# Performance work log

Measured on AMD Instinct MI355X. Metric: run time of the kernel, lower is better.

## Reference

```python
import jax, jax.numpy as jnp
import numpy as np

NUM_EXPERTS = 8
TOP_K = 2
HIDDEN = 2048
INTER = 7168
B, S = 4, 2048


def setup_inputs() -> dict:
    key = jax.random.key(0)
    k0, k1, k2, k3, k4 = jax.random.split(key, 5)
    scale_h = 1.0 / np.sqrt(HIDDEN)
    scale_i = 1.0 / np.sqrt(INTER)
    return {
        "hidden_states": jax.random.normal(k0, (B, S, HIDDEN), dtype=jnp.float32),
        "gate_w": jax.random.normal(k1, (NUM_EXPERTS, HIDDEN), dtype=jnp.float32) * scale_h,
        "w1": jax.random.normal(k2, (NUM_EXPERTS, INTER, HIDDEN), dtype=jnp.float32) * scale_h,
        "w3": jax.random.normal(k3, (NUM_EXPERTS, INTER, HIDDEN), dtype=jnp.float32) * scale_h,
        "w2": jax.random.normal(k4, (NUM_EXPERTS, HIDDEN, INTER), dtype=jnp.float32) * scale_i,
    }


def reference(hidden_states, gate_w, w1, w3, w2):
    orig_shape = hidden_states.shape
    x = hidden_states.reshape(-1, HIDDEN)              # [T, H]

    # Router: gate linear -> softmax -> top-k -> renormalize.
    router_logits = x @ gate_w.T                       # [T, E]
    probs = jax.nn.softmax(router_logits, axis=-1)
    topk_w, topk_idx = jax.lax.top_k(probs, TOP_K)     # [T, K]
    topk_w = topk_w / jnp.sum(topk_w, axis=-1, keepdims=True)

    # Dense combine weights: [T, E] with top-k renormalized weights scattered.
    combine = jnp.sum(
        jax.nn.one_hot(topk_idx, NUM_EXPERTS, dtype=x.dtype) * topk_w[..., None],
        axis=1,
    )                                                   # [T, E]

    out = jnp.zeros_like(x)
    # Fixed small loop over experts (structurally distinct weight matrices);
    # avoids materializing a [T, E, I] intermediate.
    for e in range(NUM_EXPERTS):
        g = jax.nn.silu(x @ w1[e].T)                   # [T, I]
        u = x @ w3[e].T                                # [T, I]
        y = (g * u) @ w2[e].T                          # [T, H]
        out = out + combine[:, e:e + 1] * y

    return out.reshape(orig_shape)
```

## Files before the change

### kernel.cpp

```cpp
#include <hip/hip_runtime.h>
#include <stdint.h>

#define NE    8
#define HID   2048
#define INTER 7168
#define TTOK  8192
#define NT1   (HID / 64)
#define NT2   (INTER / 64)

typedef __bf16 bf16;
typedef bf16 bf16x4 __attribute__((ext_vector_type(4)));
typedef bf16 bf16x8 __attribute__((ext_vector_type(8)));
typedef float f32x4 __attribute__((ext_vector_type(4)));

__device__ __forceinline__ void glds16(const void* g, void* l) {
  __builtin_amdgcn_global_load_lds((__attribute__((address_space(1))) void*)g,
                                   (__attribute__((address_space(3))) void*)l, 16, 0, 0);
}

__global__ void cvt_f32_bf16(const float* __restrict__ src, bf16* __restrict__ dst, long n) {
  long i = (long)blockIdx.x * blockDim.x + threadIdx.x;
  long stride = (long)gridDim.x * blockDim.x;
  for (long j = i * 4; j < n; j += stride * 4) {
    float4 v = *(const float4*)(src + j);
    bf16x4 o = {(bf16)v.x, (bf16)v.y, (bf16)v.z, (bf16)v.w};
    *(bf16x4*)(dst + j) = o;
  }
}

__global__ void router_kernel(const float* __restrict__ x, const float* __restrict__ gw,
                              int* __restrict__ topk_e, float* __restrict__ topk_w) {
  const int wid = threadIdx.x >> 6, lane = threadIdx.x & 63;
  const int t = blockIdx.x * 4 + wid;
  if (t >= TTOK) return;
  const float* xr = x + (size_t)t * HID;
  float xv[32];
#pragma unroll
  for (int i = 0; i < 32; ++i) xv[i] = xr[lane + 64 * i];
  float lg[NE];
#pragma unroll
  for (int e = 0; e < NE; ++e) {
    const float* g = gw + e * HID;
    float s = 0.f;
#pragma unroll
    for (int i = 0; i < 32; ++i) s += xv[i] * g[lane + 64 * i];
#pragma unroll
    for (int off = 32; off; off >>= 1) s += __shfl_down(s, off);
    lg[e] = s;
  }
  if (lane == 0) {
    int i1 = 0;
#pragma unroll
    for (int e = 1; e < NE; ++e) if (lg[e] > lg[i1]) i1 = e;
    int i2 = (i1 == 0) ? 1 : 0;
#pragma unroll
    for (int e = 0; e < NE; ++e) if (e != i2 && e != i1 && lg[e] > lg[i2]) i2 = e;
    float r = __expf(lg[i2] - lg[i1]);
    float wa = 1.f / (1.f + r);
    topk_e[2 * t] = i1; topk_e[2 * t + 1] = i2;
    topk_w[2 * t] = wa; topk_w[2 * t + 1] = 1.f - wa;
  }
}

__global__ void gather_sorted(const int* __restrict__ topk_e, const float* __restrict__ topk_w,
                              int* __restrict__ cnt, int* __restrict__ ltok,
                              float* __restrict__ lw, int* __restrict__ ppos) {
  const int e = blockIdx.x;
  const int tid = threadIdx.x;
  const int lane = tid & 63, wv = tid >> 6;
  __shared__ int wtot[4];
  __shared__ int basesh;
  if (tid == 0) basesh = 0;
  __syncthreads();
  for (int c0 = 0; c0 < TTOK; c0 += 256) {
    const int t = c0 + tid;
    const int e0 = topk_e[2 * t], e1 = topk_e[2 * t + 1];
    const int j = (e0 == e) ? 0 : 1;
    const int flag = (e0 == e) || (e1 == e);
    unsigned long long b = __ballot(flag);
    int wrank = __popcll(b & ((1ULL << lane) - 1ULL));
    if (lane == 63) wtot[wv] = __popcll(b);
    __syncthreads();
    int wbase = 0;
#pragma unroll
    for (int k = 0; k < 4; ++k) if (k < wv) wbase += wtot[k];
    const int total = wtot[0] + wtot[1] + wtot[2] + wtot[3];
    const int pos = basesh + wbase + wrank;
    if (flag) {
      ltok[e * TTOK + pos] = t;
      lw[e * TTOK + pos] = (j == 0) ? topk_w[2 * t] : topk_w[2 * t + 1];
      ppos[2 * t + j] = pos;
    }
    __syncthreads();
    if (tid == 0) basesh += total;
    __syncthreads();
  }
  if (tid == 0) cnt[e] = basesh;
}

__global__ void prefix_kernel(const int* __restrict__ cnt, int* __restrict__ base) {
  if (threadIdx.x == 0 && blockIdx.x == 0) {
    int b = 0;
    for (int e = 0; e < NE; ++e) { base[e] = b; b += cnt[e]; }
    base[NE] = b;
  }
}

__global__ void combine_kernel(const float* __restrict__ ybuf, const int* __restrict__ topk_e,
                               const int* __restrict__ ppos, const int* __restrict__ basep,
                               float* __restrict__ out) {
  const int t = blockIdx.x;
  const int col = threadIdx.x * 8;
  const int g0 = basep[topk_e[2 * t]] + ppos[2 * t];
  const int g1 = basep[topk_e[2 * t + 1]] + ppos[2 * t + 1];
  const float4* y0 = (const float4*)(ybuf + (size_t)g0 * HID + col);
  const float4* y1 = (const float4*)(ybuf + (size_t)g1 * HID + col);
  float4* o = (float4*)(out + (size_t)t * HID + col);
  float4 a0 = y0[0], b0 = y1[0];
  float4 a1 = y0[1], b1 = y1[1];
  o[0] = make_float4(a0.x + b0.x, a0.y + b0.y, a0.z + b0.z, a0.w + b0.w);
  o[1] = make_float4(a1.x + b1.x, a1.y + b1.y, a1.z + b1.z, a1.w + b1.w);
}


#define MFMA(a, b, c) __builtin_amdgcn_mfma_f32_16x16x32_bf16((a), (b), (c), 0, 0, 0)

#define STAGE_A(h, kt) do { int _b = ((kt) & 1) * 32768; size_t _k = (size_t)(kt) * 128; \
    glds16(bA + oA[(h)*2 + 0] + _k, ldsA + _b + (h) * 16384 + d0); \
    glds16(bA + oA[(h)*2 + 1] + _k, ldsA + _b + (h) * 16384 + d1); } while (0)
#define STAGE_B(h, kt) do { int _b = ((kt) & 1) * 32768; size_t _k = (size_t)(kt) * 128; \
    glds16(bB + oB[(h)*2 + 0] + _k, ldsB + _b + (h) * 16384 + d0); \
    glds16(bB + oB[(h)*2 + 1] + _k, ldsB + _b + (h) * 16384 + d1); } while (0)

#define RD_A(mf, ks) (*(const bf16x8*)(ldsA + curb + arow + (mf) * (16 * 128) + ((ks) ? kcol1 : kcol0)))
#define RD_B(nf, ks) (*(const bf16x8*)(ldsB + curb + brow + (nf) * (16 * 128) + ((ks) ? kcol1 : kcol0)))

#define BAR()    __builtin_amdgcn_s_barrier()
#define LGKMC(n) do { asm volatile("s_waitcnt lgkmcnt(" #n ")" ::: "memory"); \
                      __builtin_amdgcn_sched_barrier(0); } while (0)
#define SCHED0() __builtin_amdgcn_sched_barrier(0)

#define Q_MFMA(AM, BM, ACCM, ACCN_OFF) do { \
  __builtin_amdgcn_s_setprio(1); \
  _Pragma("unroll") \
  for (int m = 0; m < 4; ++m) \
    _Pragma("unroll") \
    for (int n = 0; n < 2; ++n) { \
      acc[ACCM + m][ACCN_OFF + n] = MFMA(AM[m][0], BM[n][0], acc[ACCM + m][ACCN_OFF + n]); \
      acc[ACCM + m][ACCN_OFF + n] = MFMA(AM[m][1], BM[n][1], acc[ACCM + m][ACCN_OFF + n]); \
    } \
  __builtin_amdgcn_s_setprio(0); \
} while (0)

__launch_bounds__(512, 2)
__global__ void pass1_kernel(const bf16* __restrict__ xb, const bf16* __restrict__ w1b,
                             bf16* __restrict__ hbuf, const int* __restrict__ cnt,
                             const int* __restrict__ basep, const int* __restrict__ ltok) {
  const int e = blockIdx.z;
  const int c = cnt[e];
  const int tm = blockIdx.y;
  if (tm * 256 >= c) return;
  const int tn = blockIdx.x;

  __shared__ __align__(16) bf16 sA[2][256 * 64];
  __shared__ __align__(16) bf16 sB[2][256 * 64];
  char* const ldsA = (char*)&sA[0][0];
  char* const ldsB = (char*)&sB[0][0];

  const int tid = threadIdx.x;
  const int r0 = tid >> 3;
  const int ls = (tid & 7) ^ (r0 & 7);
  const int d0 = tid * 16, d1 = (tid + 512) * 16;
  const char* const bA = (const char*)xb;
  const char* const bB = (const char*)w1b;

  uint32_t oA[4], oB[4];
#pragma unroll
  for (int i = 0; i < 4; ++i) {
    int trow = i * 64 + r0;
    int slot = tm * 256 + trow; if (slot >= c) slot = c - 1;
    oA[i] = (uint32_t)((size_t)ltok[e * TTOK + slot] * (HID * 2) + ls * 16);
    int br = i * 64 + r0;
    int w = (br >> 4) & 1;
    int wr = tn * 128 + ((br >> 5) << 4) + (br & 15);
    size_t off = ((size_t)e * INTER + wr) * (HID * 2) + (size_t)ls * 16;
    if (w) off += (size_t)NE * INTER * HID * 2;
    oB[i] = (uint32_t)off;
  }

  const int lane = tid & 63, wid = tid >> 6;
  const int wm = wid >> 2, wn = wid & 3;
  const int ln15 = lane & 15, kq = lane >> 4;
  const int swz = (ln15 & 7) << 4;
  const int kcol0 = (kq * 16) ^ swz;
  const int kcol1 = (64 + kq * 16) ^ swz;
  const int arow = (wm * 128 + ln15) * 128;
  const int brow = (wn * 64 + ln15) * 128;

  f32x4 acc[8][4];
#pragma unroll
  for (int m = 0; m < 8; ++m)
#pragma unroll
    for (int n = 0; n < 4; ++n) acc[m][n] = (f32x4){0.f, 0.f, 0.f, 0.f};

  STAGE_A(0, 0); STAGE_A(1, 0); STAGE_B(0, 0); STAGE_B(1, 0);
  asm volatile("s_waitcnt vmcnt(4)" ::: "memory");
  STAGE_A(0, 1); STAGE_A(1, 1); STAGE_B(0, 1);
  asm volatile("s_waitcnt vmcnt(6)" ::: "memory");
  BAR();

  bf16x8 a0[4][2], a1[4][2], b0[2][2], b1[2][2];
  int cur = 0;
  for (int t = 0; t < NT1; ++t, cur ^= 1) {
    const int curb = cur * 32768;
#pragma unroll
    for (int m = 0; m < 4; ++m) { a0[m][0] = RD_A(m, 0); a0[m][1] = RD_A(m, 1); }
#pragma unroll
    for (int n = 0; n < 2; ++n) { b0[n][0] = RD_B(n, 0); b0[n][1] = RD_B(n, 1); }
    if (t + 1 < NT1) STAGE_B(1, t + 1);
    BAR(); LGKMC(12);
    if (t > 0) Q_MFMA(a1, b1, 4, 2);
    BAR();
#pragma unroll
    for (int m = 0; m < 4; ++m) { a1[m][0] = RD_A(4 + m, 0); a1[m][1] = RD_A(4 + m, 1); }
    BAR(); LGKMC(8);
    Q_MFMA(a0, b0, 0, 0);
    BAR();
#pragma unroll
    for (int n = 0; n < 2; ++n) { b1[n][0] = RD_B(2 + n, 0); b1[n][1] = RD_B(2 + n, 1); }
    if (t + 2 < NT1) { STAGE_A(0, t + 2); STAGE_A(1, t + 2); SCHED0(); }
    BAR(); LGKMC(4);
    Q_MFMA(a1, b0, 4, 0);
    BAR();
    if (t + 2 < NT1) STAGE_B(0, t + 2);
    LGKMC(0);
    Q_MFMA(a0, b1, 0, 2);
    if (t + 2 < NT1) asm volatile("s_waitcnt vmcnt(6)" ::: "memory");
    else             asm volatile("s_waitcnt vmcnt(0)" ::: "memory");
    BAR();
  }
  Q_MFMA(a1, b1, 4, 2);

  const int be = basep[e];
#pragma unroll
  for (int mh = 0; mh < 2; ++mh)
#pragma unroll
    for (int mf = 0; mf < 4; ++mf)
#pragma unroll
      for (int j = 0; j < 4; ++j) {
        const int slot = tm * 256 + wm * 128 + mh * 64 + mf * 16 + kq * 4 + j;
        if (slot < c) {
          bf16* hrow = hbuf + (size_t)(be + slot) * INTER + tn * 128;
#pragma unroll
          for (int p = 0; p < 2; ++p) {
            const float g = acc[mh * 4 + mf][2 * p][j];
            const float u = acc[mh * 4 + mf][2 * p + 1][j];
            const float hv = g / (1.f + __expf(-g)) * u;
            hrow[wn * 32 + p * 16 + ln15] = (bf16)hv;
          }
        }
      }
}

__launch_bounds__(512, 2)
__global__ void pass2_kernel(const bf16* __restrict__ hbuf, const bf16* __restrict__ w2b,
                             float* __restrict__ ybuf, const int* __restrict__ cnt,
                             const int* __restrict__ basep, const float* __restrict__ lw) {
  const int e = blockIdx.z;
  const int c = cnt[e];
  const int tm = blockIdx.y;
  if (tm * 256 >= c) return;
  const int tn = blockIdx.x;

  __shared__ __align__(16) bf16 sA[2][256 * 64];
  __shared__ __align__(16) bf16 sB[2][256 * 64];
  char* const ldsA = (char*)&sA[0][0];
  char* const ldsB = (char*)&sB[0][0];

  const int tid = threadIdx.x;
  const int r0 = tid >> 3;
  const int ls = (tid & 7) ^ (r0 & 7);
  const int d0 = tid * 16, d1 = (tid + 512) * 16;
  const int be = basep[e];
  const char* const bA = (const char*)hbuf;
  const char* const bB = (const char*)w2b;

  uint32_t oA[4], oB[4];
#pragma unroll
  for (int i = 0; i < 4; ++i) {
    int trow = i * 64 + r0;
    int slot = tm * 256 + trow; if (slot >= c) slot = c - 1;
    oA[i] = (uint32_t)((size_t)(be + slot) * (INTER * 2) + ls * 16);
    oB[i] = (uint32_t)(((size_t)e * HID + tn * 256 + i * 64 + r0) * (INTER * 2) + (size_t)ls * 16);
  }

  const int lane = tid & 63, wid = tid >> 6;
  const int wm = wid >> 2, wn = wid & 3;
  const int ln15 = lane & 15, kq = lane >> 4;
  const int swz = (ln15 & 7) << 4;
  const int kcol0 = (kq * 16) ^ swz;
  const int kcol1 = (64 + kq * 16) ^ swz;
  const int arow = (wm * 128 + ln15) * 128;
  const int brow = (wn * 64 + ln15) * 128;

  f32x4 acc[8][4];
#pragma unroll
  for (int m = 0; m < 8; ++m)
#pragma unroll
    for (int n = 0; n < 4; ++n) acc[m][n] = (f32x4){0.f, 0.f, 0.f, 0.f};

  STAGE_A(0, 0); STAGE_A(1, 0); STAGE_B(0, 0); STAGE_B(1, 0);
  asm volatile("s_waitcnt vmcnt(4)" ::: "memory");
  STAGE_A(0, 1); STAGE_A(1, 1); STAGE_B(0, 1);
  asm volatile("s_waitcnt vmcnt(6)" ::: "memory");
  BAR();

  bf16x8 a0[4][2], a1[4][2], b0[2][2], b1[2][2];
  int cur = 0;
  for (int t = 0; t < NT2; ++t, cur ^= 1) {
    const int curb = cur * 32768;
#pragma unroll
    for (int m = 0; m < 4; ++m) { a0[m][0] = RD_A(m, 0); a0[m][1] = RD_A(m, 1); }
#pragma unroll
    for (int n = 0; n < 2; ++n) { b0[n][0] = RD_B(n, 0); b0[n][1] = RD_B(n, 1); }
    if (t + 1 < NT2) STAGE_B(1, t + 1);
    BAR(); LGKMC(12);
    if (t > 0) Q_MFMA(a1, b1, 4, 2);
    BAR();
#pragma unroll
    for (int m = 0; m < 4; ++m) { a1[m][0] = RD_A(4 + m, 0); a1[m][1] = RD_A(4 + m, 1); }
    BAR(); LGKMC(8);
    Q_MFMA(a0, b0, 0, 0);
    BAR();
#pragma unroll
    for (int n = 0; n < 2; ++n) { b1[n][0] = RD_B(2 + n, 0); b1[n][1] = RD_B(2 + n, 1); }
    if (t + 2 < NT2) { STAGE_A(0, t + 2); STAGE_A(1, t + 2); SCHED0(); }
    BAR(); LGKMC(4);
    Q_MFMA(a1, b0, 4, 0);
    BAR();
    if (t + 2 < NT2) STAGE_B(0, t + 2);
    LGKMC(0);
    Q_MFMA(a0, b1, 0, 2);
    if (t + 2 < NT2) asm volatile("s_waitcnt vmcnt(6)" ::: "memory");
    else             asm volatile("s_waitcnt vmcnt(0)" ::: "memory");
    BAR();
  }
  Q_MFMA(a1, b1, 4, 2);

#pragma unroll
  for (int mh = 0; mh < 2; ++mh)
#pragma unroll
    for (int mf = 0; mf < 4; ++mf)
#pragma unroll
      for (int j = 0; j < 4; ++j) {
        const int slot = tm * 256 + wm * 128 + mh * 64 + mf * 16 + kq * 4 + j;
        if (slot < c) {
          const float wt = lw[e * TTOK + slot];
          float* yrow = ybuf + (size_t)(be + slot) * HID + tn * 256;
#pragma unroll
          for (int n = 0; n < 4; ++n)
            yrow[wn * 64 + n * 16 + ln15] = wt * acc[mh * 4 + mf][n][j];
        }
      }
}

extern "C" void kernel_launch(void* const* d_in, const int* in_sizes, int n_in,
                              void* d_out, int out_size, void* d_ws, size_t ws_size,
                              hipStream_t stream) {
  const float* x  = (const float*)d_in[0];
  const float* gw = (const float*)d_in[1];
  const float* w1 = (const float*)d_in[2];
  const float* w3 = (const float*)d_in[3];
  const float* w2 = (const float*)d_in[4];
  float* out = (float*)d_out;

  char* ws = (char*)d_ws;
  size_t off = 0;
  auto take = [&](size_t bytes) -> char* {
    char* p = ws + off;
    off += (bytes + 255) & ~(size_t)255;
    return p;
  };
  bf16* xb    = (bf16*)take((size_t)TTOK * HID * 2);
  bf16* w1b   = (bf16*)take((size_t)NE * INTER * HID * 2);
  bf16* w3b   = (bf16*)take((size_t)NE * INTER * HID * 2);
  bf16* w2b   = (bf16*)take((size_t)NE * HID * INTER * 2);
  bf16* hbuf  = (bf16*)take((size_t)TTOK * 2 * INTER * 2);
  float* ybuf = (float*)take((size_t)TTOK * 2 * HID * 4);
  int*   topk_e = (int*)take(TTOK * 2 * 4);
  float* topk_w = (float*)take(TTOK * 2 * 4);
  int*   ltok   = (int*)take(NE * TTOK * 4);
  float* lwgt   = (float*)take(NE * TTOK * 4);
  int*   ppos   = (int*)take(TTOK * 2 * 4);
  int*   cntp   = (int*)take(64);
  int*   basep  = (int*)take(64);
  if (off > ws_size) return;

  cvt_f32_bf16<<<2048, 256, 0, stream>>>(x,  xb,  (long)TTOK * HID);
  cvt_f32_bf16<<<4096, 256, 0, stream>>>(w1, w1b, (long)NE * INTER * HID);
  cvt_f32_bf16<<<4096, 256, 0, stream>>>(w3, w3b, (long)NE * INTER * HID);
  cvt_f32_bf16<<<4096, 256, 0, stream>>>(w2, w2b, (long)NE * HID * INTER);

  router_kernel<<<TTOK / 4, 256, 0, stream>>>(x, gw, topk_e, topk_w);
  gather_sorted<<<NE, 256, 0, stream>>>(topk_e, topk_w, cntp, ltok, lwgt, ppos);
  prefix_kernel<<<1, 64, 0, stream>>>(cntp, basep);

  pass1_kernel<<<dim3(INTER / 128, TTOK / 256, NE), 512, 0, stream>>>(
      xb, w1b, hbuf, cntp, basep, ltok);
  pass2_kernel<<<dim3(HID / 256, TTOK / 256, NE), 512, 0, stream>>>(
      hbuf, w2b, ybuf, cntp, basep, lwgt);
  combine_kernel<<<TTOK, 256, 0, stream>>>(ybuf, topk_e, ppos, basep, out);
}
```

Baseline: 2.103 ms.

## Merge conversion kernels, fuse x cast into router, drop prefix kernel, bf16 ybuf

The three weight-conversion launches become a single kernel that indexes w1b/w3b/w2b as contiguous segments. The activation cast to bf16 moves into the router kernel. The prefix-sum kernel is removed and each consumer recomputes expert base offsets from the counts. The per-slot expert output buffer now stores bf16 instead of fp32, halving its write and read traffic in pass2 and combine, at the cost of an extra rounding step before the final sum.

```diff
diff --git a/kernel.cpp b/kernel.cpp
--- a/kernel.cpp
+++ b/kernel.cpp
@@ -18,25 +18,35 @@
                                    (__attribute__((address_space(3))) void*)l, 16, 0, 0);
 }
 
-__global__ void cvt_f32_bf16(const float* __restrict__ src, bf16* __restrict__ dst, long n) {
-  long i = (long)blockIdx.x * blockDim.x + threadIdx.x;
-  long stride = (long)gridDim.x * blockDim.x;
-  for (long j = i * 4; j < n; j += stride * 4) {
+__global__ void cvt3_kernel(const float* __restrict__ s0, const float* __restrict__ s1,
+                            const float* __restrict__ s2, bf16* __restrict__ dst) {
+  const long SEG = (long)NE * INTER * HID;
+  const int seg = blockIdx.x >> 12;
+  const int bid = blockIdx.x & 4095;
+  const float* src = (seg == 0) ? s0 : ((seg == 1) ? s1 : s2);
+  bf16* d = dst + (size_t)seg * SEG;
+  long i = (long)bid * blockDim.x + threadIdx.x;
+  const long stride = (long)4096 * blockDim.x;
+  for (long j = i * 4; j < SEG; j += stride * 4) {
     float4 v = *(const float4*)(src + j);
     bf16x4 o = {(bf16)v.x, (bf16)v.y, (bf16)v.z, (bf16)v.w};
-    *(bf16x4*)(dst + j) = o;
+    *(bf16x4*)(d + j) = o;
   }
 }
 
 __global__ void router_kernel(const float* __restrict__ x, const float* __restrict__ gw,
+                              bf16* __restrict__ xb,
                               int* __restrict__ topk_e, float* __restrict__ topk_w) {
   const int wid = threadIdx.x >> 6, lane = threadIdx.x & 63;
   const int t = blockIdx.x * 4 + wid;
   if (t >= TTOK) return;
   const float* xr = x + (size_t)t * HID;
+  bf16* xw = xb + (size_t)t * HID;
   float xv[32];
 #pragma unroll
   for (int i = 0; i < 32; ++i) xv[i] = xr[lane + 64 * i];
+#pragma unroll
+  for (int i = 0; i < 32; ++i) xw[lane + 64 * i] = (bf16)xv[i];
   float lg[NE];
 #pragma unroll
   for (int e = 0; e < NE; ++e) {
@@ -98,28 +108,29 @@
   if (tid == 0) cnt[e] = basesh;
 }
 
-__global__ void prefix_kernel(const int* __restrict__ cnt, int* __restrict__ base) {
-  if (threadIdx.x == 0 && blockIdx.x == 0) {
+__global__ void combine_kernel(const bf16* __restrict__ ybuf, const int* __restrict__ topk_e,
+                               const int* __restrict__ ppos, const int* __restrict__ cnt,
+                               float* __restrict__ out) {
+  __shared__ int pref[NE];
+  if (threadIdx.x < NE) {
     int b = 0;
-    for (int e = 0; e < NE; ++e) { base[e] = b; b += cnt[e]; }
-    base[NE] = b;
-  }
-}
-
-__global__ void combine_kernel(const float* __restrict__ ybuf, const int* __restrict__ topk_e,
-                               const int* __restrict__ ppos, const int* __restrict__ basep,
-                               float* __restrict__ out) {
+    for (int k = 0; k < (int)threadIdx.x; ++k) b += cnt[k];
+    pref[threadIdx.x] = b;
+  }
+  __syncthreads();
   const int t = blockIdx.x;
   const int col = threadIdx.x * 8;
-  const int g0 = basep[topk_e[2 * t]] + ppos[2 * t];
-  const int g1 = basep[topk_e[2 * t + 1]] + ppos[2 * t + 1];
-  const float4* y0 = (const float4*)(ybuf + (size_t)g0 * HID + col);
-  const float4* y1 = (const float4*)(ybuf + (size_t)g1 * HID + col);
+  const int g0 = pref[topk_e[2 * t]] + ppos[2 * t];
+  const int g1 = pref[topk_e[2 * t + 1]] + ppos[2 * t + 1];
+  bf16x8 y0 = *(const bf16x8*)(ybuf + (size_t)g0 * HID + col);
+  bf16x8 y1 = *(const bf16x8*)(ybuf + (size_t)g1 * HID + col);
+  float4 o0, o1;
+  o0.x = (float)y0[0] + (float)y1[0]; o0.y = (float)y0[1] + (float)y1[1];
+  o0.z = (float)y0[2] + (float)y1[2]; o0.w = (float)y0[3] + (float)y1[3];
+  o1.x = (float)y0[4] + (float)y1[4]; o1.y = (float)y0[5] + (float)y1[5];
+  o1.z = (float)y0[6] + (float)y1[6]; o1.w = (float)y0[7] + (float)y1[7];
   float4* o = (float4*)(out + (size_t)t * HID + col);
-  float4 a0 = y0[0], b0 = y1[0];
-  float4 a1 = y0[1], b1 = y1[1];
-  o[0] = make_float4(a0.x + b0.x, a0.y + b0.y, a0.z + b0.z, a0.w + b0.w);
-  o[1] = make_float4(a1.x + b1.x, a1.y + b1.y, a1.z + b1.z, a1.w + b1.w);
+  o[0] = o0; o[1] = o1;
 }
 
 
@@ -155,12 +166,15 @@
 __launch_bounds__(512, 2)
 __global__ void pass1_kernel(const bf16* __restrict__ xb, const bf16* __restrict__ w1b,
                              bf16* __restrict__ hbuf, const int* __restrict__ cnt,
-                             const int* __restrict__ basep, const int* __restrict__ ltok) {
+                             const int* __restrict__ ltok) {
   const int e = blockIdx.z;
   const int c = cnt[e];
   const int tm = blockIdx.y;
   if (tm * 256 >= c) return;
   const int tn = blockIdx.x;
+  int be = 0;
+#pragma unroll
+  for (int k = 0; k < NE; ++k) if (k < e) be += cnt[k];
 
   __shared__ __align__(16) bf16 sA[2][256 * 64];
   __shared__ __align__(16) bf16 sB[2][256 * 64];
@@ -177,8 +191,7 @@
   uint32_t oA[4], oB[4];
 #pragma unroll
   for (int i = 0; i < 4; ++i) {
-    int trow = i * 64 + r0;
-    int slot = tm * 256 + trow; if (slot >= c) slot = c - 1;
+    int slot = tm * 256 + i * 64 + r0; if (slot >= c) slot = c - 1;
     oA[i] = (uint32_t)((size_t)ltok[e * TTOK + slot] * (HID * 2) + ls * 16);
     int br = i * 64 + r0;
     int w = (br >> 4) & 1;
@@ -241,7 +254,6 @@
   }
   Q_MFMA(a1, b1, 4, 2);
 
-  const int be = basep[e];
 #pragma unroll
   for (int mh = 0; mh < 2; ++mh)
 #pragma unroll
@@ -264,13 +276,16 @@
 
 __launch_bounds__(512, 2)
 __global__ void pass2_kernel(const bf16* __restrict__ hbuf, const bf16* __restrict__ w2b,
-                             float* __restrict__ ybuf, const int* __restrict__ cnt,
-                             const int* __restrict__ basep, const float* __restrict__ lw) {
+                             bf16* __restrict__ ybuf, const int* __restrict__ cnt,
+                             const float* __restrict__ lw) {
   const int e = blockIdx.z;
   const int c = cnt[e];
   const int tm = blockIdx.y;
   if (tm * 256 >= c) return;
   const int tn = blockIdx.x;
+  int be = 0;
+#pragma unroll
+  for (int k = 0; k < NE; ++k) if (k < e) be += cnt[k];
 
   __shared__ __align__(16) bf16 sA[2][256 * 64];
   __shared__ __align__(16) bf16 sB[2][256 * 64];
@@ -281,15 +296,13 @@
   const int r0 = tid >> 3;
   const int ls = (tid & 7) ^ (r0 & 7);
   const int d0 = tid * 16, d1 = (tid + 512) * 16;
-  const int be = basep[e];
   const char* const bA = (const char*)hbuf;
   const char* const bB = (const char*)w2b;
 
   uint32_t oA[4], oB[4];
 #pragma unroll
   for (int i = 0; i < 4; ++i) {
-    int trow = i * 64 + r0;
-    int slot = tm * 256 + trow; if (slot >= c) slot = c - 1;
+    int slot = tm * 256 + i * 64 + r0; if (slot >= c) slot = c - 1;
     oA[i] = (uint32_t)((size_t)(be + slot) * (INTER * 2) + ls * 16);
     oB[i] = (uint32_t)(((size_t)e * HID + tn * 256 + i * 64 + r0) * (INTER * 2) + (size_t)ls * 16);
   }
@@ -356,10 +369,10 @@
         const int slot = tm * 256 + wm * 128 + mh * 64 + mf * 16 + kq * 4 + j;
         if (slot < c) {
           const float wt = lw[e * TTOK + slot];
-          float* yrow = ybuf + (size_t)(be + slot) * HID + tn * 256;
+          bf16* yrow = ybuf + (size_t)(be + slot) * HID + tn * 256;
 #pragma unroll
           for (int n = 0; n < 4; ++n)
-            yrow[wn * 64 + n * 16 + ln15] = wt * acc[mh * 4 + mf][n][j];
+            yrow[wn * 64 + n * 16 + ln15] = (bf16)(wt * acc[mh * 4 + mf][n][j]);
         }
       }
 }
@@ -386,28 +399,24 @@
   bf16* w3b   = (bf16*)take((size_t)NE * INTER * HID * 2);
   bf16* w2b   = (bf16*)take((size_t)NE * HID * INTER * 2);
   bf16* hbuf  = (bf16*)take((size_t)TTOK * 2 * INTER * 2);
-  float* ybuf = (float*)take((size_t)TTOK * 2 * HID * 4);
+  bf16* ybuf  = (bf16*)take((size_t)TTOK * 2 * HID * 2);
   int*   topk_e = (int*)take(TTOK * 2 * 4);
   float* topk_w = (float*)take(TTOK * 2 * 4);
   int*   ltok   = (int*)take(NE * TTOK * 4);
   float* lwgt   = (float*)take(NE * TTOK * 4);
   int*   ppos   = (int*)take(TTOK * 2 * 4);
   int*   cntp   = (int*)take(64);
-  int*   basep  = (int*)take(64);
   if (off > ws_size) return;
-
-  cvt_f32_bf16<<<2048, 256, 0, stream>>>(x,  xb,  (long)TTOK * HID);
-  cvt_f32_bf16<<<4096, 256, 0, stream>>>(w1, w1b, (long)NE * INTER * HID);
-  cvt_f32_bf16<<<4096, 256, 0, stream>>>(w3, w3b, (long)NE * INTER * HID);
-  cvt_f32_bf16<<<4096, 256, 0, stream>>>(w2, w2b, (long)NE * HID * INTER);
-
-  router_kernel<<<TTOK / 4, 256, 0, stream>>>(x, gw, topk_e, topk_w);
+  (void)w3b; (void)w2b;
+
+  cvt3_kernel<<<3 * 4096, 256, 0, stream>>>(w1, w3, w2, w1b);
+
+  router_kernel<<<TTOK / 4, 256, 0, stream>>>(x, gw, xb, topk_e, topk_w);
   gather_sorted<<<NE, 256, 0, stream>>>(topk_e, topk_w, cntp, ltok, lwgt, ppos);
-  prefix_kernel<<<1, 64, 0, stream>>>(cntp, basep);
 
   pass1_kernel<<<dim3(INTER / 128, TTOK / 256, NE), 512, 0, stream>>>(
-      xb, w1b, hbuf, cntp, basep, ltok);
+      xb, w1b, hbuf, cntp, ltok);
   pass2_kernel<<<dim3(HID / 256, TTOK / 256, NE), 512, 0, stream>>>(
-      hbuf, w2b, ybuf, cntp, basep, lwgt);
-  combine_kernel<<<TTOK, 256, 0, stream>>>(ybuf, topk_e, ppos, basep, out);
-}
+      hbuf, w2b, ybuf, cntp, lwgt);
+  combine_kernel<<<TTOK, 256, 0, stream>>>(ybuf, topk_e, ppos, cntp, out);
+}
```

Result: no change. 2.106 ms, median of 2 (+0.1%).
